# Optimization experiments

Hardware: AMD Instinct MI355X
Metric: run time of the kernel (lower is better)

The kernel has to match this reference:

```python
import jax, jax.numpy as jnp
import numpy as np

NUM_HEADS = 16
EPS = 1e-6

def _rmsnorm(h, w):
    h32 = h.astype(jnp.float32)
    var = jnp.mean(h32 * h32, axis=-1, keepdims=True)
    return (w * (h32 * jax.lax.rsqrt(var + EPS))).astype(h.dtype)

def setup_inputs() -> dict:
    key = jax.random.key(0)
    ks = jax.random.split(key, 4)
    B, N, C = 16, 1024, 1024
    x = jax.random.normal(ks[0], (B, N, C), dtype=jnp.float32)
    qkv_w = jax.random.normal(ks[1], (3 * C, C), dtype=jnp.float32) * (C ** -0.5)
    proj_w = jax.random.normal(ks[2], (C, C), dtype=jnp.float32) * (C ** -0.5)
    proj_b = jnp.zeros((C,), dtype=jnp.float32)
    q_norm_w = jnp.ones((C // NUM_HEADS,), dtype=jnp.float32)
    k_norm_w = jnp.ones((C // NUM_HEADS,), dtype=jnp.float32)
    return {"x": x, "qkv_w": qkv_w, "proj_w": proj_w, "proj_b": proj_b,
            "q_norm_w": q_norm_w, "k_norm_w": k_norm_w}

def reference(x, qkv_w, proj_w, proj_b, q_norm_w, k_norm_w):
    B, N, C = x.shape
    H = NUM_HEADS
    Dh = C // H
    scale = Dh ** -0.5  # qk_scale default; temperature = 1.0
    # QKV projection (no bias): [B,N,3,H,Dh]
    qkv = (x @ qkv_w.T).reshape(B, N, 3, H, Dh)
    q, k, v = qkv[:, :, 0], qkv[:, :, 1], qkv[:, :, 2]
    # per-head QK RMSNorm (fp32 internally)
    q = _rmsnorm(q, q_norm_w)
    k = _rmsnorm(k, k_norm_w)
    # explicit softmax attention: [B,H,N,N]
    attn = jnp.einsum('bnhd,bmhd->bhnm', q * scale, k)
    attn = jax.nn.softmax(attn, axis=-1)
    out = jnp.einsum('bhnm,bmhd->bnhd', attn, v).reshape(B, N, C)
    return out @ proj_w.T + proj_b
```

## Files before the change

kernel.cpp:

```cpp
#include <hip/hip_runtime.h>
#include <hip/hip_bf16.h>

typedef __attribute__((ext_vector_type(8))) __bf16 bf16x8;
typedef __attribute__((ext_vector_type(4))) __bf16 bf16x4;
typedef __attribute__((ext_vector_type(4))) float f32x4;

#define AS1(p) ((__attribute__((address_space(1))) void*)(p))
#define AS3(p) ((__attribute__((address_space(3))) void*)(p))

__global__ void f2b_kernel(const float4* __restrict__ in, bf16x4* __restrict__ out, int n4) {
    int idx = blockIdx.x * blockDim.x + threadIdx.x;
    int stride = gridDim.x * blockDim.x;
    for (int i = idx; i < n4; i += stride) {
        float4 v = in[i];
        bf16x4 o;
        o[0] = (__bf16)v.x; o[1] = (__bf16)v.y; o[2] = (__bf16)v.z; o[3] = (__bf16)v.w;
        out[i] = o;
    }
}

template<int MODE>
__global__ __launch_bounds__(512, 2)
void gemm256(const __bf16* __restrict__ A, const __bf16* __restrict__ Bw,
             const float* __restrict__ bias, const float* __restrict__ qw,
             const float* __restrict__ kw, float* __restrict__ Cf,
             __bf16* __restrict__ Cb, __bf16* __restrict__ Vt,
             int M, int K, int nbn, int ldc)
{
    __shared__ __bf16 Asl[4][256 * 32];
    __shared__ __bf16 Bsl[4][256 * 32];
    const int tid = threadIdx.x, l = tid & 63, w = tid >> 6;
    const int fr = l & 15, fk = l >> 4;

    const int cpx = gridDim.x >> 3;
    const int wg = (blockIdx.x & 7) * cpx + (blockIdx.x >> 3);
    const int bm = wg / nbn, bn = wg % nbn;

    const __bf16* Ag = A + (size_t)bm * 256 * K;
    const __bf16* Bg = Bw + (size_t)bn * 256 * K;

    const int arow = tid >> 2;
    const int uch = (tid & 3) ^ ((arow >> 1) & 3);
    const size_t ga = (size_t)arow * K + uch * 8;
    const size_t ga2 = ga + (size_t)128 * K;

    const int axc = (fk ^ ((fr >> 1) & 3)) * 16;
    int aoff[8], boff[4];
    #pragma unroll
    for (int m = 0; m < 8; ++m)
        aoff[m] = ((w >> 2) * 128 + m * 16 + fr) * 64 + axc;
    #pragma unroll
    for (int n = 0; n < 4; ++n)
        boff[n] = ((w & 3) * 64 + n * 16 + fr) * 64 + axc;

    f32x4 acc[8][4] = {};

#define STAGE256(S) do {                                                                    \
    const int sb_ = (S) & 3;                                                                \
    __builtin_amdgcn_global_load_lds(AS1(Ag + (size_t)(S) * 32 + ga),                       \
        AS3((char*)&Asl[sb_][0] + tid * 16), 16, 0, 0);                                     \
    __builtin_amdgcn_global_load_lds(AS1(Ag + (size_t)(S) * 32 + ga2),                      \
        AS3((char*)&Asl[sb_][0] + tid * 16 + 8192), 16, 0, 0);                              \
    __builtin_amdgcn_global_load_lds(AS1(Bg + (size_t)(S) * 32 + ga),                       \
        AS3((char*)&Bsl[sb_][0] + tid * 16), 16, 0, 0);                                     \
    __builtin_amdgcn_global_load_lds(AS1(Bg + (size_t)(S) * 32 + ga2),                      \
        AS3((char*)&Bsl[sb_][0] + tid * 16 + 8192), 16, 0, 0);                              \
} while (0)

#define PHASE256(S, VMSTR, DOSTAGE) do {                                                    \
    asm volatile("s_waitcnt vmcnt(" VMSTR ")" ::: "memory");                                \
    __builtin_amdgcn_s_barrier();                                                           \
    __builtin_amdgcn_sched_barrier(0);                                                      \
    const int pb_ = (S) & 3;                                                                \
    bf16x8 af[8], bfv[4];                                                                   \
    _Pragma("unroll")                                                                       \
    for (int m = 0; m < 8; ++m)                                                             \
        af[m] = *(const bf16x8*)((const char*)&Asl[pb_][0] + aoff[m]);                      \
    _Pragma("unroll")                                                                       \
    for (int n = 0; n < 4; ++n)                                                             \
        bfv[n] = *(const bf16x8*)((const char*)&Bsl[pb_][0] + boff[n]);                     \
    if (DOSTAGE) STAGE256((S) + 3);                                                         \
    __builtin_amdgcn_s_setprio(1);                                                          \
    _Pragma("unroll")                                                                       \
    for (int m = 0; m < 8; ++m)                                                             \
        _Pragma("unroll")                                                                   \
        for (int n = 0; n < 4; ++n)                                                         \
            acc[m][n] = __builtin_amdgcn_mfma_f32_16x16x32_bf16(af[m], bfv[n], acc[m][n], 0, 0, 0); \
    __builtin_amdgcn_s_setprio(0);                                                          \
} while (0)

    const int S = K >> 5;
    STAGE256(0); STAGE256(1); STAGE256(2);
    for (int s = 0; s < S - 2; ++s)
        PHASE256(s, "8", (s + 3 < S));
    PHASE256(S - 2, "4", false);
    PHASE256(S - 1, "0", false);
#undef PHASE256
#undef STAGE256

    const int rb0 = bm * 256 + (w >> 2) * 128 + fk * 4;
    const int cb0 = bn * 256 + (w & 3) * 64;

    if (MODE == 1) {
        #pragma unroll
        for (int m = 0; m < 8; ++m)
            #pragma unroll
            for (int n = 0; n < 4; ++n) {
                const int col = cb0 + n * 16 + fr;
                const float bv = bias[col];
                #pragma unroll
                for (int r = 0; r < 4; ++r)
                    Cf[(size_t)(rb0 + m * 16 + r) * ldc + col] = acc[m][n][r] + bv;
            }
    } else {
        const int sect = bn >> 2;
        if (sect < 2) {
            const float* wp = (sect == 0) ? qw : kw;
            float wn[4];
            #pragma unroll
            for (int n = 0; n < 4; ++n) wn[n] = wp[((w & 3) * 64 + n * 16 + fr) & 63];
            #pragma unroll
            for (int m = 0; m < 8; ++m) {
                float sc[4];
                #pragma unroll
                for (int r = 0; r < 4; ++r) {
                    float ps = 0.f;
                    #pragma unroll
                    for (int n = 0; n < 4; ++n) ps += acc[m][n][r] * acc[m][n][r];
                    ps += __shfl_xor(ps, 1); ps += __shfl_xor(ps, 2);
                    ps += __shfl_xor(ps, 4); ps += __shfl_xor(ps, 8);
                    sc[r] = rsqrtf(ps * (1.0f / 64.0f) + 1e-6f);
                    if (sect == 0) sc[r] *= 0.18033688011112042f;
                }
                #pragma unroll
                for (int n = 0; n < 4; ++n)
                    #pragma unroll
                    for (int r = 0; r < 4; ++r)
                        Cb[(size_t)(rb0 + m * 16 + r) * ldc + cb0 + n * 16 + fr] =
                            (__bf16)(acc[m][n][r] * sc[r] * wn[n]);
            }
        } else {
            #pragma unroll
            for (int m = 0; m < 8; ++m) {
                const int tok = rb0 + m * 16;
                const int b = tok >> 10, ntok = tok & 1023;
                #pragma unroll
                for (int n = 0; n < 4; ++n) {
                    const int vd = (bn - 8) * 256 + (w & 3) * 64 + n * 16 + fr;
                    bf16x4 pk;
                    #pragma unroll
                    for (int r = 0; r < 4; ++r) pk[r] = (__bf16)acc[m][n][r];
                    *(bf16x4*)&Vt[((size_t)((b * 16 + (vd >> 6)) * 64 + (vd & 63))) * 1024 + ntok] = pk;
                }
            }
        }
    }
}

__global__ __launch_bounds__(256, 2)
void attn_kernel(const __bf16* __restrict__ qkv, const __bf16* __restrict__ vt,
                 __bf16* __restrict__ ao)
{
    __shared__ __bf16 Ks[4][64 * 64];
    __shared__ __bf16 Vs[4][64 * 64];
    __shared__ __bf16 Pl[4][16 * 64];
    const int tid = threadIdx.x, l = tid & 63, w = tid >> 6;
    const int fr = l & 15, fk = l >> 4;
    const int sw = (fr & 7) << 4;

    const int bi = blockIdx.x;
    const int L = (bi & 7) * 128 + (bi >> 3);
    const int qb = L & 3, h = (L >> 2) & 15, b = L >> 6;

    const __bf16* Kg = qkv + (size_t)b * 1024 * 2048 + 1024 + h * 64;
    const __bf16* Vg = vt + (size_t)((b * 16 + h) * 64) * 1024;
    const int srow = tid >> 3, scp = tid & 7;

    const int c8 = (scp ^ (srow & 7)) * 8;
    const size_t kO0 = (size_t)srow * 2048 + c8, kO1 = kO0 + 32 * 2048;
    const size_t vO0 = (size_t)srow * 1024 + c8, vO1 = vO0 + 32 * 1024;
    char* ksd = (char*)&Ks[0][0] + tid * 16;
    char* vsd = (char*)&Vs[0][0] + tid * 16;

#define STAGE(KT) do {                                                                    \
    char* dk_ = ksd + ((KT) & 3) * 8192;                                                  \
    char* dv_ = vsd + ((KT) & 3) * 8192;                                                  \
    __builtin_amdgcn_global_load_lds(AS1(Kg + (size_t)(KT) * 131072 + kO0), AS3(dk_), 16, 0, 0); \
    __builtin_amdgcn_global_load_lds(AS1(Kg + (size_t)(KT) * 131072 + kO1), AS3(dk_ + 4096), 16, 0, 0); \
    __builtin_amdgcn_global_load_lds(AS1(Vg + (KT) * 64 + vO0), AS3(dv_), 16, 0, 0);      \
    __builtin_amdgcn_global_load_lds(AS1(Vg + (KT) * 64 + vO1), AS3(dv_ + 4096), 16, 0, 0); \
} while (0)

    STAGE(0); STAGE(1);

    const int qrow0 = b * 1024 + qb * 256 + w * 64;
    bf16x8 qf[4][2];
    #pragma unroll
    for (int qi = 0; qi < 4; ++qi)
        #pragma unroll
        for (int dc = 0; dc < 2; ++dc)
            qf[qi][dc] = *(const bf16x8*)&qkv[(size_t)(qrow0 + qi * 16 + fr) * 2048
                                              + h * 64 + dc * 32 + fk * 8];

    const int kb0 = fr * 128 + ((fk ^ (fr & 7)) * 16);
    const int kb1 = fr * 128 + (((4 + fk) ^ (fr & 7)) * 16);
    const char* KsB = (const char*)&Ks[0][0];
    const char* VsB = (const char*)&Vs[0][0];

    char* Pw = (char*)&Pl[w][0];
    const int pw0 = (fr * 128 + 0 * 32 + fk * 8) ^ sw;
    const int pw1 = (fr * 128 + 1 * 32 + fk * 8) ^ sw;
    const int pw2 = (fr * 128 + 2 * 32 + fk * 8) ^ sw;
    const int pw3 = (fr * 128 + 3 * 32 + fk * 8) ^ sw;
    const int pr0 = (fr * 128 + 0 * 64 + fk * 16) ^ sw;
    const int pr1 = (fr * 128 + 1 * 64 + fk * 16) ^ sw;

    bf16x8 onesf;
    #pragma unroll
    for (int i = 0; i < 8; ++i) onesf[i] = (__bf16)1.0f;

    f32x4 oacc[4][4] = {};
    f32x4 lacc[4] = {};

    for (int p = 0; p < 8; ++p) {
        asm volatile("s_waitcnt vmcnt(0)" ::: "memory");
        __builtin_amdgcn_s_barrier();
        __builtin_amdgcn_sched_barrier(0);
        if (p < 7) { STAGE(2 * p + 2); STAGE(2 * p + 3); }

        #pragma unroll
        for (int kh = 0; kh < 2; ++kh) {
            const int cb = (((p & 1) << 1) | kh) * 8192;
            bf16x8 kf[4][2], vf[4][2];
            #pragma unroll
            for (int n = 0; n < 4; ++n) {
                kf[n][0] = *(const bf16x8*)(KsB + cb + kb0 + n * 2048);
                kf[n][1] = *(const bf16x8*)(KsB + cb + kb1 + n * 2048);
            }
            #pragma unroll
            for (int nd = 0; nd < 4; ++nd) {
                vf[nd][0] = *(const bf16x8*)(VsB + cb + kb0 + nd * 2048);
                vf[nd][1] = *(const bf16x8*)(VsB + cb + kb1 + nd * 2048);
            }

            #pragma unroll
            for (int qi = 0; qi < 4; ++qi) {
                f32x4 sacc[4] = {};
                #pragma unroll
                for (int n = 0; n < 4; ++n)
                    #pragma unroll
                    for (int dc = 0; dc < 2; ++dc)
                        sacc[n] = __builtin_amdgcn_mfma_f32_16x16x32_bf16(kf[n][dc], qf[qi][dc],
                                                                          sacc[n], 0, 0, 0);

                #pragma unroll
                for (int n = 0; n < 4; ++n) {
                    bf16x4 pk;
                    #pragma unroll
                    for (int r = 0; r < 4; ++r)
                        pk[r] = (__bf16)__builtin_amdgcn_exp2f(sacc[n][r]);
                    const int pwn = (n == 0) ? pw0 : (n == 1) ? pw1 : (n == 2) ? pw2 : pw3;
                    *(bf16x4*)(Pw + pwn) = pk;
                }

                bf16x8 pf0 = *(const bf16x8*)(Pw + pr0);
                bf16x8 pf1 = *(const bf16x8*)(Pw + pr1);
                lacc[qi] = __builtin_amdgcn_mfma_f32_16x16x32_bf16(pf0, onesf, lacc[qi], 0, 0, 0);
                lacc[qi] = __builtin_amdgcn_mfma_f32_16x16x32_bf16(pf1, onesf, lacc[qi], 0, 0, 0);
                #pragma unroll
                for (int nd = 0; nd < 4; ++nd) {
                    oacc[qi][nd] = __builtin_amdgcn_mfma_f32_16x16x32_bf16(pf0, vf[nd][0],
                                                                           oacc[qi][nd], 0, 0, 0);
                    oacc[qi][nd] = __builtin_amdgcn_mfma_f32_16x16x32_bf16(pf1, vf[nd][1],
                                                                           oacc[qi][nd], 0, 0, 0);
                }
            }
        }
    }

    #pragma unroll
    for (int qi = 0; qi < 4; ++qi) {
        float inv[4];
        #pragma unroll
        for (int r = 0; r < 4; ++r)
            inv[r] = __builtin_amdgcn_rcpf(lacc[qi][r]);
        #pragma unroll
        for (int nd = 0; nd < 4; ++nd)
            #pragma unroll
            for (int r = 0; r < 4; ++r)
                ao[(size_t)(qrow0 + qi * 16 + fk * 4 + r) * 1024 + h * 64 + nd * 16 + fr] =
                    (__bf16)(oacc[qi][nd][r] * inv[r]);
    }
#undef STAGE
}

extern "C" void kernel_launch(void* const* d_in, const int* in_sizes, int n_in,
                              void* d_out, int out_size, void* d_ws, size_t ws_size,
                              hipStream_t stream)
{
    const float* x      = (const float*)d_in[0];
    const float* qkv_w  = (const float*)d_in[1];
    const float* proj_w = (const float*)d_in[2];
    const float* proj_b = (const float*)d_in[3];
    const float* qnw    = (const float*)d_in[4];
    const float* knw    = (const float*)d_in[5];

    char* ws = (char*)d_ws;
    __bf16* xb    = (__bf16*)(ws);
    __bf16* wqkv  = (__bf16*)(ws + 33554432);
    __bf16* wproj = (__bf16*)(ws + 39845888);
    __bf16* qkv   = (__bf16*)(ws + 41943040);
    __bf16* vt    = (__bf16*)(ws + 109051904);
    __bf16* ao    = (__bf16*)(ws + 142606336);

    f2b_kernel<<<2048, 256, 0, stream>>>((const float4*)x,      (bf16x4*)xb,    16777216 / 4);
    f2b_kernel<<<2048, 256, 0, stream>>>((const float4*)qkv_w,  (bf16x4*)wqkv,  3145728 / 4);
    f2b_kernel<<<1024, 256, 0, stream>>>((const float4*)proj_w, (bf16x4*)wproj, 1048576 / 4);

    gemm256<0><<<768, 512, 0, stream>>>(xb, wqkv, nullptr, qnw, knw,
                                        nullptr, qkv, vt, 16384, 1024, 12, 2048);
    attn_kernel<<<1024, 256, 0, stream>>>(qkv, vt, ao);
    gemm256<1><<<256, 512, 0, stream>>>(ao, wproj, proj_b, nullptr, nullptr,
                                        (float*)d_out, nullptr, nullptr, 16384, 1024, 4, 1024);
}
```

Measured before the change: 254.1 us.

## Split QKV GEMM into dedicated 4-wave kernel with 128x128 warp tiles

The QKV projection moves from the shared 8-wave template GEMM into its own 256-thread kernel. Each wave now computes a 128x128 sub-tile (8x8 MFMA accumulators), and LDS fragments are double-buffered in registers so the next k-slice is read while the current MFMAs run. The goal is more MFMA work per LDS read and less barrier overhead per FLOP. In exchange it uses many more registers (256 accumulator floats per lane) and runs one block per CU, which lowers occupancy and latency hiding; the RMSNorm epilogue is adjusted to handle two heads per wave.

```diff
diff --git a/kernel.cpp b/kernel.cpp
--- a/kernel.cpp
+++ b/kernel.cpp
@@ -19,13 +19,149 @@
     }
 }
 
-template<int MODE>
+__global__ __launch_bounds__(256, 1)
+void gemmqkv(const __bf16* __restrict__ A, const __bf16* __restrict__ Bw,
+             const float* __restrict__ qw, const float* __restrict__ kw,
+             __bf16* __restrict__ Cb, __bf16* __restrict__ Vt,
+             int K, int nbn, int ldc)
+{
+    __shared__ __bf16 Asl[4][256 * 32];
+    __shared__ __bf16 Bsl[4][256 * 32];
+    const int tid = threadIdx.x, l = tid & 63, w = tid >> 6;
+    const int fr = l & 15, fk = l >> 4;
+
+    const int cpx = gridDim.x >> 3;
+    const int wg = (blockIdx.x & 7) * cpx + (blockIdx.x >> 3);
+    const int bm = wg / nbn, bn = wg % nbn;
+
+    const __bf16* Ag = A + (size_t)bm * 256 * K;
+    const __bf16* Bg = Bw + (size_t)bn * 256 * K;
+
+    const size_t ga = (size_t)(tid >> 2) * K + (((tid & 3) ^ ((tid >> 3) & 3)) * 8);
+    char* const AsB = (char*)&Asl[0][0];
+    char* const BsB = (char*)&Bsl[0][0];
+
+    const int axc = (fk ^ ((fr >> 1) & 3)) * 16;
+    int aoff[8], boff[8];
+    #pragma unroll
+    for (int m = 0; m < 8; ++m)
+        aoff[m] = ((w >> 1) * 128 + m * 16 + fr) * 64 + axc;
+    #pragma unroll
+    for (int n = 0; n < 8; ++n)
+        boff[n] = ((w & 1) * 128 + n * 16 + fr) * 64 + axc;
+
+    f32x4 acc[8][8] = {};
+    bf16x8 a0[8], b0[8], a1[8], b1[8];
+
+#define STAGEQ(S) do {                                                                      \
+    const int sb_ = (S) & 3;                                                                \
+    _Pragma("unroll")                                                                       \
+    for (int i_ = 0; i_ < 4; ++i_) {                                                        \
+        __builtin_amdgcn_global_load_lds(AS1(Ag + (size_t)(S) * 32 + (size_t)i_ * 64 * K + ga), \
+            AS3(AsB + sb_ * 16384 + i_ * 4096 + tid * 16), 16, 0, 0);                       \
+        __builtin_amdgcn_global_load_lds(AS1(Bg + (size_t)(S) * 32 + (size_t)i_ * 64 * K + ga), \
+            AS3(BsB + sb_ * 16384 + i_ * 4096 + tid * 16), 16, 0, 0);                       \
+    } } while (0)
+
+#define SLOTQ(S, AU, BU, AF, BF) do {                                                       \
+    asm volatile("s_waitcnt vmcnt(8)" ::: "memory");                                        \
+    __builtin_amdgcn_s_barrier();                                                           \
+    __builtin_amdgcn_sched_barrier(0);                                                      \
+    if ((S) + 1 < 32) {                                                                     \
+        const int nb_ = ((S) + 1) & 3;                                                      \
+        _Pragma("unroll")                                                                   \
+        for (int m = 0; m < 8; ++m)                                                         \
+            AF[m] = *(const bf16x8*)(AsB + nb_ * 16384 + aoff[m]);                          \
+        _Pragma("unroll")                                                                   \
+        for (int n = 0; n < 8; ++n)                                                         \
+            BF[n] = *(const bf16x8*)(BsB + nb_ * 16384 + boff[n]);                          \
+    }                                                                                       \
+    if ((S) + 3 < 32) STAGEQ((S) + 3);                                                      \
+    __builtin_amdgcn_s_setprio(1);                                                          \
+    _Pragma("unroll")                                                                       \
+    for (int m = 0; m < 8; ++m)                                                             \
+        _Pragma("unroll")                                                                   \
+        for (int n = 0; n < 8; ++n)                                                         \
+            acc[m][n] = __builtin_amdgcn_mfma_f32_16x16x32_bf16(AU[m], BU[n], acc[m][n], 0, 0, 0); \
+    __builtin_amdgcn_s_setprio(0);                                                          \
+} while (0)
+
+    STAGEQ(0); STAGEQ(1); STAGEQ(2);
+    asm volatile("s_waitcnt vmcnt(16)" ::: "memory");
+    __builtin_amdgcn_s_barrier();
+    #pragma unroll
+    for (int m = 0; m < 8; ++m) a0[m] = *(const bf16x8*)(AsB + aoff[m]);
+    #pragma unroll
+    for (int n = 0; n < 8; ++n) b0[n] = *(const bf16x8*)(BsB + boff[n]);
+
+    for (int s = 0; s < 32; s += 2) {
+        SLOTQ(s, a0, b0, a1, b1);
+        SLOTQ(s + 1, a1, b1, a0, b0);
+    }
+#undef SLOTQ
+#undef STAGEQ
+
+    const int rb0 = bm * 256 + (w >> 1) * 128 + fk * 4;
+    const int cb0 = bn * 256 + (w & 1) * 128;
+    const int sect = bn >> 2;
+
+    if (sect < 2) {
+        const float* wp = (sect == 0) ? qw : kw;
+        float wn[8];
+        #pragma unroll
+        for (int n = 0; n < 8; ++n) wn[n] = wp[(n * 16 + fr) & 63];
+        #pragma unroll
+        for (int m = 0; m < 8; ++m) {
+            float scA[4], scB[4];
+            #pragma unroll
+            for (int r = 0; r < 4; ++r) {
+                float psA = 0.f, psB = 0.f;
+                #pragma unroll
+                for (int n = 0; n < 4; ++n) {
+                    psA += acc[m][n][r] * acc[m][n][r];
+                    psB += acc[m][4 + n][r] * acc[m][4 + n][r];
+                }
+                psA += __shfl_xor(psA, 1); psA += __shfl_xor(psA, 2);
+                psA += __shfl_xor(psA, 4); psA += __shfl_xor(psA, 8);
+                psB += __shfl_xor(psB, 1); psB += __shfl_xor(psB, 2);
+                psB += __shfl_xor(psB, 4); psB += __shfl_xor(psB, 8);
+                scA[r] = rsqrtf(psA * (1.0f / 64.0f) + 1e-6f);
+                scB[r] = rsqrtf(psB * (1.0f / 64.0f) + 1e-6f);
+                if (sect == 0) {
+                    scA[r] *= 0.18033688011112042f;
+                    scB[r] *= 0.18033688011112042f;
+                }
+            }
+            #pragma unroll
+            for (int n = 0; n < 8; ++n) {
+                const float* sc = (n < 4) ? scA : scB;
+                #pragma unroll
+                for (int r = 0; r < 4; ++r)
+                    Cb[(size_t)(rb0 + m * 16 + r) * ldc + cb0 + n * 16 + fr] =
+                        (__bf16)(acc[m][n][r] * sc[r] * wn[n]);
+            }
+        }
+    } else {
+        #pragma unroll
+        for (int m = 0; m < 8; ++m) {
+            const int tok = rb0 + m * 16;
+            const int b = tok >> 10, ntok = tok & 1023;
+            #pragma unroll
+            for (int n = 0; n < 8; ++n) {
+                const int vd = (bn - 8) * 256 + (w & 1) * 128 + n * 16 + fr;
+                bf16x4 pk;
+                #pragma unroll
+                for (int r = 0; r < 4; ++r) pk[r] = (__bf16)acc[m][n][r];
+                *(bf16x4*)&Vt[((size_t)((b * 16 + (vd >> 6)) * 64 + (vd & 63))) * 1024 + ntok] = pk;
+            }
+        }
+    }
+}
+
 __global__ __launch_bounds__(512, 2)
-void gemm256(const __bf16* __restrict__ A, const __bf16* __restrict__ Bw,
-             const float* __restrict__ bias, const float* __restrict__ qw,
-             const float* __restrict__ kw, float* __restrict__ Cf,
-             __bf16* __restrict__ Cb, __bf16* __restrict__ Vt,
-             int M, int K, int nbn, int ldc)
+void gemm_proj(const __bf16* __restrict__ A, const __bf16* __restrict__ Bw,
+               const float* __restrict__ bias, float* __restrict__ Cf,
+               int K, int nbn, int ldc)
 {
     __shared__ __bf16 Asl[4][256 * 32];
     __shared__ __bf16 Bsl[4][256 * 32];
@@ -100,61 +236,16 @@
 
     const int rb0 = bm * 256 + (w >> 2) * 128 + fk * 4;
     const int cb0 = bn * 256 + (w & 3) * 64;
-
-    if (MODE == 1) {
-        #pragma unroll
-        for (int m = 0; m < 8; ++m)
-            #pragma unroll
-            for (int n = 0; n < 4; ++n) {
-                const int col = cb0 + n * 16 + fr;
-                const float bv = bias[col];
-                #pragma unroll
-                for (int r = 0; r < 4; ++r)
-                    Cf[(size_t)(rb0 + m * 16 + r) * ldc + col] = acc[m][n][r] + bv;
-            }
-    } else {
-        const int sect = bn >> 2;
-        if (sect < 2) {
-            const float* wp = (sect == 0) ? qw : kw;
-            float wn[4];
-            #pragma unroll
-            for (int n = 0; n < 4; ++n) wn[n] = wp[((w & 3) * 64 + n * 16 + fr) & 63];
-            #pragma unroll
-            for (int m = 0; m < 8; ++m) {
-                float sc[4];
-                #pragma unroll
-                for (int r = 0; r < 4; ++r) {
-                    float ps = 0.f;
-                    #pragma unroll
-                    for (int n = 0; n < 4; ++n) ps += acc[m][n][r] * acc[m][n][r];
-                    ps += __shfl_xor(ps, 1); ps += __shfl_xor(ps, 2);
-                    ps += __shfl_xor(ps, 4); ps += __shfl_xor(ps, 8);
-                    sc[r] = rsqrtf(ps * (1.0f / 64.0f) + 1e-6f);
-                    if (sect == 0) sc[r] *= 0.18033688011112042f;
-                }
-                #pragma unroll
-                for (int n = 0; n < 4; ++n)
-                    #pragma unroll
-                    for (int r = 0; r < 4; ++r)
-                        Cb[(size_t)(rb0 + m * 16 + r) * ldc + cb0 + n * 16 + fr] =
-                            (__bf16)(acc[m][n][r] * sc[r] * wn[n]);
-            }
-        } else {
-            #pragma unroll
-            for (int m = 0; m < 8; ++m) {
-                const int tok = rb0 + m * 16;
-                const int b = tok >> 10, ntok = tok & 1023;
-                #pragma unroll
-                for (int n = 0; n < 4; ++n) {
-                    const int vd = (bn - 8) * 256 + (w & 3) * 64 + n * 16 + fr;
-                    bf16x4 pk;
-                    #pragma unroll
-                    for (int r = 0; r < 4; ++r) pk[r] = (__bf16)acc[m][n][r];
-                    *(bf16x4*)&Vt[((size_t)((b * 16 + (vd >> 6)) * 64 + (vd & 63))) * 1024 + ntok] = pk;
-                }
-            }
+    #pragma unroll
+    for (int m = 0; m < 8; ++m)
+        #pragma unroll
+        for (int n = 0; n < 4; ++n) {
+            const int col = cb0 + n * 16 + fr;
+            const float bv = bias[col];
+            #pragma unroll
+            for (int r = 0; r < 4; ++r)
+                Cf[(size_t)(rb0 + m * 16 + r) * ldc + col] = acc[m][n][r] + bv;
         }
-    }
 }
 
 __global__ __launch_bounds__(256, 2)
@@ -317,9 +408,7 @@
     f2b_kernel<<<2048, 256, 0, stream>>>((const float4*)qkv_w,  (bf16x4*)wqkv,  3145728 / 4);
     f2b_kernel<<<1024, 256, 0, stream>>>((const float4*)proj_w, (bf16x4*)wproj, 1048576 / 4);
 
-    gemm256<0><<<768, 512, 0, stream>>>(xb, wqkv, nullptr, qnw, knw,
-                                        nullptr, qkv, vt, 16384, 1024, 12, 2048);
+    gemmqkv<<<768, 256, 0, stream>>>(xb, wqkv, qnw, knw, qkv, vt, 1024, 12, 2048);
     attn_kernel<<<1024, 256, 0, stream>>>(qkv, vt, ao);
-    gemm256<1><<<256, 512, 0, stream>>>(ao, wproj, proj_b, nullptr, nullptr,
-                                        (float*)d_out, nullptr, nullptr, 16384, 1024, 4, 1024);
+    gemm_proj<<<256, 512, 0, stream>>>(ao, wproj, proj_b, (float*)d_out, 1024, 4, 1024);
 }
```

New measurement: 772.4 us. 3.04x slower.
